# Kernel tuning notes

Measured on AMD Instinct MI355X. Metric: run time of the kernel, lower is better.

Reference implementation:

```python
import jax, jax.numpy as jnp
import numpy as np

MAX_EDGE_LENGTH = 100.0  # filtration cap from cfg['self_supervised']['max_edge_length']


def pairwise_dist(x):
    # Euclidean pairwise distances, [N, N]
    sq = jnp.sum(x * x, axis=-1)
    d2 = sq[:, None] + sq[None, :] - 2.0 * (x @ x.T)
    return jnp.sqrt(jnp.maximum(d2, 0.0) + 1e-12)


def mst_edge_weights(D):
    """Prim's MST over dense distance matrix D [N,N]. Returns N-1 edge weights.
    These weights are exactly the H0 death times of the Vietoris-Rips filtration
    (all H0 features are born at 0)."""
    N = D.shape[0]
    dist0 = D[0]                                   # min distance from tree to each node
    in_tree0 = jnp.zeros((N,), bool).at[0].set(True)

    def step(carry, _):
        dist, in_tree = carry
        masked = jnp.where(in_tree, jnp.inf, dist)
        j = jnp.argmin(masked)
        w = masked[j]                              # weight of edge added to MST
        in_tree = in_tree.at[j].set(True)
        dist = jnp.minimum(dist, D[j])
        return (dist, in_tree), w

    _, weights = jax.lax.scan(step, (dist0, in_tree0), None, length=N - 1)
    return weights


def h0_deaths(x):
    # H0 persistence diagram deaths (births are all 0), capped at max_edge_length
    return jnp.minimum(mst_edge_weights(pairwise_dist(x)), MAX_EDGE_LENGTH)


def setup_inputs() -> dict:
    key = jax.random.key(0)
    k1, k2 = jax.random.split(key)
    N, Dm = 4096, 128
    x_1 = jax.random.normal(k1, (N, Dm), dtype=jnp.float32)
    # correlated second view, as in a siamese/self-supervised setting
    x_2 = x_1 + 0.1 * jax.random.normal(k2, (N, Dm), dtype=jnp.float32)
    return {"x_1": x_1, "x_2": x_2, "plot": 0}


def reference(x_1, x_2, plot):
    # MSE representation loss
    representation_loss = jnp.mean((x_1 - x_2) ** 2)
    # H0 persistence diagrams via Vietoris-Rips (MST formulation)
    d1 = jnp.sort(h0_deaths(x_1))
    d2 = jnp.sort(h0_deaths(x_2))
    # Wasserstein-1 distance between the two H0 diagrams (births all 0,
    # equal cardinality => optimal matching is the sorted matching of deaths)
    topological_loss = jnp.sum(jnp.abs(d1 - d2))
    return representation_loss + topological_loss
```

## Files before the change

### kernel.cpp

```cpp
#include <hip/hip_runtime.h>
#include <hip/hip_fp16.h>

#define NPT 4096
#define DM 128
#define ROUNDS 12
#define INF64 0xFFFFFFFFFFFFFFFFull

typedef _Float16 f16x8 __attribute__((ext_vector_type(8)));
typedef _Float16 f16x2 __attribute__((ext_vector_type(2)));
typedef float f32x4 __attribute__((ext_vector_type(4)));

__global__ __launch_bounds__(256) void init_kernel(unsigned* __restrict__ comp,
                                                   unsigned long long* __restrict__ compbest,
                                                   float* __restrict__ w,
                                                   unsigned* __restrict__ cnt,
                                                   float* __restrict__ rep) {
    int i = blockIdx.x * blockDim.x + threadIdx.x;
    comp[i] = (unsigned)(i & (NPT - 1));
    compbest[i] = INF64;
    w[i] = 0.0f;
    if (i < 2) cnt[i] = 0u;
    if (i == 0) rep[0] = 0.0f;
}

__global__ __launch_bounds__(256) void prep_kernel(const float* __restrict__ x1,
                                                   const float* __restrict__ x2,
                                                   _Float16* __restrict__ Xh,
                                                   float* __restrict__ norms) {
    const int wv = threadIdx.x >> 6, ln = threadIdx.x & 63;
    const int row = blockIdx.x * 4 + wv;
    const float* src = (row < NPT) ? (x1 + (size_t)row * DM)
                                   : (x2 + (size_t)(row - NPT) * DM);
    float2 v = *(const float2*)(src + ln * 2);
    _Float16 h0 = (_Float16)v.x, h1 = (_Float16)v.y;
    f16x2 p; p[0] = h0; p[1] = h1;
    *(f16x2*)(Xh + (size_t)row * DM + ln * 2) = p;
    float a = (float)h0, b = (float)h1;
    float s = a * a + b * b;
    #pragma unroll
    for (int off = 32; off > 0; off >>= 1) s += __shfl_down(s, off);
    if (ln == 0) norms[row] = s;
}

__global__ __launch_bounds__(256) void gram_kernel(const _Float16* __restrict__ Xh,
                                                   const float* __restrict__ norms,
                                                   __half* __restrict__ Dall) {
    const int mat = blockIdx.y;
    const _Float16* __restrict__ X = Xh + (size_t)mat * NPT * DM;
    const float* __restrict__ nrm = norms + mat * NPT;
    __half* __restrict__ D = Dall + (size_t)mat * NPT * NPT;

    const int I = blockIdx.x >> 5;
    const int J = blockIdx.x & 31;

    __shared__ _Float16 tile[128 * 136];

    const int t = threadIdx.x;
    const int wv = t >> 6, ln = t & 63;
    const int rloc = (wv >> 1) * 64;
    const int cloc = (wv & 1) * 64;
    const int rowBase = I * 128 + rloc;
    const int colBase = J * 128 + cloc;
    const int lr = ln & 15;
    const int kg = ln >> 4;

    f32x4 acc[4][4];
    #pragma unroll
    for (int m = 0; m < 4; ++m)
        #pragma unroll
        for (int n = 0; n < 4; ++n)
            acc[m][n] = (f32x4){0.f, 0.f, 0.f, 0.f};

    #pragma unroll
    for (int ks = 0; ks < 4; ++ks) {
        const int k0 = ks * 32 + kg * 8;
        f16x8 a[4], b[4];
        #pragma unroll
        for (int m = 0; m < 4; ++m)
            a[m] = *(const f16x8*)(X + (size_t)(rowBase + m * 16 + lr) * DM + k0);
        #pragma unroll
        for (int n = 0; n < 4; ++n)
            b[n] = *(const f16x8*)(X + (size_t)(colBase + n * 16 + lr) * DM + k0);
        #pragma unroll
        for (int m = 0; m < 4; ++m)
            #pragma unroll
            for (int n = 0; n < 4; ++n)
                acc[m][n] = __builtin_amdgcn_mfma_f32_16x16x32_f16(a[m], b[n], acc[m][n], 0, 0, 0);
    }

    float nr[16], nc[4];
    #pragma unroll
    for (int m = 0; m < 4; ++m)
        #pragma unroll
        for (int q = 0; q < 4; ++q)
            nr[m * 4 + q] = nrm[rowBase + m * 16 + kg * 4 + q];
    #pragma unroll
    for (int n = 0; n < 4; ++n) nc[n] = nrm[colBase + n * 16 + lr];

    #pragma unroll
    for (int m = 0; m < 4; ++m) {
        #pragma unroll
        for (int n = 0; n < 4; ++n) {
            #pragma unroll
            for (int q = 0; q < 4; ++q) {
                const int rl = rloc + m * 16 + kg * 4 + q;
                const int cl = cloc + n * 16 + lr;
                float d2 = nr[m * 4 + q] + nc[n] - 2.0f * acc[m][n][q];
                float d = sqrtf(fmaxf(d2, 0.0f) + 1e-12f);
                tile[rl * 136 + cl] = (_Float16)d;
            }
        }
    }
    __syncthreads();

    const int tileRow0 = I * 128;
    #pragma unroll
    for (int it = 0; it < 8; ++it) {
        int idx = it * 256 + t;
        int row = idx >> 4;
        int ch = idx & 15;
        *(uint4*)(&D[(size_t)(tileRow0 + row) * NPT + J * 128 + ch * 8]) =
            *(const uint4*)(&tile[row * 136 + ch * 8]);
    }
}

__global__ __launch_bounds__(1024) void boruvka_a(const __half* __restrict__ Dall,
                                                  const unsigned* __restrict__ compAll,
                                                  unsigned long long* __restrict__ compbestAll,
                                                  const unsigned* __restrict__ cnt) {
    const int mat = blockIdx.y;
    if (cnt[mat] >= NPT - 1u) return;
    const __half* __restrict__ D = Dall + (size_t)mat * NPT * NPT;
    const unsigned* __restrict__ comp = compAll + mat * NPT;
    unsigned long long* __restrict__ compbest = compbestAll + mat * NPT;

    __shared__ unsigned short lcomp[NPT];
    const int t = threadIdx.x;
    for (int i = t; i < NPT; i += 1024) lcomp[i] = (unsigned short)comp[i];
    __syncthreads();

    const int wv = t >> 6, ln = t & 63;
    const int node = blockIdx.x * 16 + wv;
    const unsigned ci = lcomp[node];
    const unsigned* __restrict__ row = (const unsigned*)(D + (size_t)node * NPT);

    unsigned best = 0xFFFFFFFFu;
    #pragma unroll
    for (int k = 0; k < 8; ++k) {
        const int jb = k * 512 + ln * 8;
        uint4 dv = *(const uint4*)(row + (jb >> 1));
        uint4 cv = *(const uint4*)&lcomp[jb];
        const unsigned dp[4] = {dv.x, dv.y, dv.z, dv.w};
        const unsigned cp[4] = {cv.x, cv.y, cv.z, cv.w};
        #pragma unroll
        for (int q = 0; q < 4; ++q) {
            int j0 = jb + q * 2;
            unsigned k0 = (dp[q] << 16) | (unsigned)j0;
            unsigned k1 = (dp[q] & 0xFFFF0000u) | (unsigned)(j0 + 1);
            if ((cp[q] & 0xFFFFu) == ci) k0 = 0xFFFFFFFFu;
            if ((cp[q] >> 16) == ci)     k1 = 0xFFFFFFFFu;
            unsigned m = k0 < k1 ? k0 : k1;
            best = best < m ? best : m;
        }
    }
    #pragma unroll
    for (int off = 32; off > 0; off >>= 1) {
        unsigned o = __shfl_down(best, off);
        best = best < o ? best : o;
    }
    if (ln == 0 && best != 0xFFFFFFFFu) {
        unsigned h = best >> 16;
        unsigned j = best & 0xFFFFu;
        unsigned mn = (unsigned)node < j ? (unsigned)node : j;
        unsigned mx = (unsigned)node < j ? j : (unsigned)node;
        unsigned long long key64 = ((unsigned long long)h << 48) |
                                   ((unsigned long long)mn << 32) |
                                   ((unsigned long long)mx << 16) |
                                   (unsigned long long)j;
        atomicMin(&compbest[ci], key64);
    }
}

__global__ __launch_bounds__(1024) void boruvka_cd(unsigned* __restrict__ compAll,
                                                   unsigned long long* __restrict__ compbestAll,
                                                   float* __restrict__ wAll,
                                                   unsigned* __restrict__ cntAll) {
    const int mat = blockIdx.x;
    if (cntAll[mat] >= NPT - 1u) return;
    unsigned* __restrict__ comp = compAll + mat * NPT;
    unsigned long long* __restrict__ compbest = compbestAll + mat * NPT;
    float* __restrict__ w = wAll + mat * NPT;
    unsigned* __restrict__ cnt = cntAll + mat;

    __shared__ unsigned short par[NPT];
    const int t = threadIdx.x;

    for (int c = t; c < NPT; c += 1024) {
        unsigned p = (unsigned)c;
        unsigned long long key = compbest[c];
        if (comp[c] == (unsigned)c && key != INF64) {
            unsigned jout = (unsigned)(key & 0xFFFFull);
            unsigned c2 = comp[jout];
            unsigned long long k2 = compbest[c2];
            bool mutual = (k2 >> 16) == (key >> 16);
            if (!mutual || (unsigned)c < c2) {
                unsigned short hb = (unsigned short)(key >> 48);
                float wv = fminf(__half2float(__ushort_as_half(hb)), 100.0f);
                unsigned slot = atomicAdd(cnt, 1u);
                w[slot] = wv;
            }
            p = (mutual && (unsigned)c < c2) ? (unsigned)c : c2;
        }
        par[c] = (unsigned short)p;
    }
    __syncthreads();

    for (int it = 0; it < 12; ++it) {
        unsigned short np[4];
        #pragma unroll
        for (int q = 0; q < 4; ++q) np[q] = par[par[t + q * 1024]];
        __syncthreads();
        #pragma unroll
        for (int q = 0; q < 4; ++q) par[t + q * 1024] = np[q];
        __syncthreads();
    }

    for (int c = t; c < NPT; c += 1024) {
        comp[c] = par[comp[c]];
        compbest[c] = INF64;
    }
}

__global__ __launch_bounds__(256) void rep_kernel(const float4* __restrict__ x1,
                                                  const float4* __restrict__ x2,
                                                  float* __restrict__ acc) {
    int idx = blockIdx.x * blockDim.x + threadIdx.x;
    int stride = gridDim.x * blockDim.x;
    float s = 0.f;
    for (int i = idx; i < NPT * DM / 4; i += stride) {
        float4 a = x1[i], b = x2[i];
        float d0 = a.x - b.x, d1 = a.y - b.y, d2 = a.z - b.z, d3 = a.w - b.w;
        s += d0 * d0 + d1 * d1 + d2 * d2 + d3 * d3;
    }
    #pragma unroll
    for (int off = 32; off > 0; off >>= 1) s += __shfl_down(s, off);
    __shared__ float partial[4];
    int wv = threadIdx.x >> 6, ln = threadIdx.x & 63;
    if (ln == 0) partial[wv] = s;
    __syncthreads();
    if (threadIdx.x == 0) {
        float tot = partial[0] + partial[1] + partial[2] + partial[3];
        atomicAdd(acc, tot);
    }
}

__global__ __launch_bounds__(1024) void sort_kernel(float* __restrict__ wAll) {
    float* __restrict__ w = wAll + blockIdx.x * NPT;
    __shared__ float s[NPT];
    const int t = threadIdx.x;
    for (int i = t; i < NPT; i += 1024) s[i] = w[i];
    __syncthreads();

    for (int k = 2; k <= NPT; k <<= 1) {
        for (int j = k >> 1; j > 0; j >>= 1) {
            for (int i = t; i < NPT; i += 1024) {
                int ixj = i ^ j;
                if (ixj > i) {
                    bool up = (i & k) == 0;
                    float a = s[i], b = s[ixj];
                    if ((a > b) == up) { s[i] = b; s[ixj] = a; }
                }
            }
            __syncthreads();
        }
    }
    for (int i = t; i < NPT; i += 1024) w[i] = s[i];
}

__global__ __launch_bounds__(1024) void final2_kernel(const float* __restrict__ w,
                                                      const float* __restrict__ rep,
                                                      float* __restrict__ out) {
    const int t = threadIdx.x;
    float loc = 0.f;
    for (int i = t; i < NPT; i += 1024) loc += fabsf(w[i] - w[NPT + i]);
    #pragma unroll
    for (int off = 32; off > 0; off >>= 1) loc += __shfl_down(loc, off);
    __shared__ float reds[16];
    int wv = t >> 6, ln = t & 63;
    if (ln == 0) reds[wv] = loc;
    __syncthreads();
    if (t == 0) {
        float tot = 0.f;
        #pragma unroll
        for (int i = 0; i < 16; ++i) tot += reds[i];
        out[0] = tot + rep[0] * (1.0f / (NPT * DM));
    }
}

extern "C" void kernel_launch(void* const* d_in, const int* in_sizes, int n_in,
                              void* d_out, int out_size, void* d_ws, size_t ws_size,
                              hipStream_t stream) {
    const float* x1 = (const float*)d_in[0];
    const float* x2 = (const float*)d_in[1];
    float* out = (float*)d_out;

    char* ws = (char*)d_ws;
    __half* D = (__half*)ws;
    size_t off = (size_t)2 * NPT * NPT * sizeof(__half);
    _Float16* Xh = (_Float16*)(ws + off);
    off += (size_t)2 * NPT * DM * sizeof(_Float16);
    float* norms = (float*)(ws + off);
    off += (size_t)2 * NPT * sizeof(float);
    unsigned long long* compbest = (unsigned long long*)(ws + off);
    off += (size_t)2 * NPT * sizeof(unsigned long long);
    float* w = (float*)(ws + off);
    off += (size_t)2 * NPT * sizeof(float);
    unsigned* comp = (unsigned*)(ws + off);
    off += (size_t)2 * NPT * sizeof(unsigned);
    unsigned* cnt = (unsigned*)(ws + off);
    off += 4 * sizeof(unsigned);
    float* rep = (float*)(ws + off);

    init_kernel<<<2 * NPT / 256, 256, 0, stream>>>(comp, compbest, w, cnt, rep);

    prep_kernel<<<2 * NPT / 4, 256, 0, stream>>>(x1, x2, Xh, norms);

    gram_kernel<<<dim3(1024, 2), 256, 0, stream>>>(Xh, norms, D);

    for (int r = 0; r < ROUNDS; ++r) {
        boruvka_a<<<dim3(NPT / 16, 2), 1024, 0, stream>>>(D, comp, compbest, cnt);
        boruvka_cd<<<2, 1024, 0, stream>>>(comp, compbest, w, cnt);
    }

    rep_kernel<<<256, 256, 0, stream>>>((const float4*)x1, (const float4*)x2, rep);

    sort_kernel<<<2, 1024, 0, stream>>>(w);

    final2_kernel<<<1, 1024, 0, stream>>>(w, rep, out);
}
```

Baseline: 340.5 us.

## Cache per-node top-8 neighbors and finish Boruvka rounds in one persistent block per matrix

The first Boruvka pass now keeps each node's eight nearest neighbors in a per-node cache instead of only the single best edge. The remaining rounds run inside one block per matrix, which uses the cache to find each component's cheapest outgoing edge. A node rescans its full distance row only when all eight cached neighbors already lie in its own component. This replaces 12 full-matrix scan rounds and 24 launches with one scan plus mostly cache lookups. The cost is that later rounds run on only two workgroups, which could serialize work if many nodes fall back to full rescans.

```diff
diff --git a/kernel.cpp b/kernel.cpp
--- a/kernel.cpp
+++ b/kernel.cpp
@@ -3,12 +3,20 @@
 
 #define NPT 4096
 #define DM 128
-#define ROUNDS 12
 #define INF64 0xFFFFFFFFFFFFFFFFull
+#define INF32 0xFFFFFFFFu
 
 typedef _Float16 f16x8 __attribute__((ext_vector_type(8)));
 typedef _Float16 f16x2 __attribute__((ext_vector_type(2)));
 typedef float f32x4 __attribute__((ext_vector_type(4)));
+
+static __device__ __forceinline__ unsigned long long make_key64(unsigned key, unsigned node) {
+    unsigned h = key >> 16, j = key & 0xFFFFu;
+    unsigned mn = node < j ? node : j;
+    unsigned mx = node < j ? j : node;
+    return ((unsigned long long)h << 48) | ((unsigned long long)mn << 32) |
+           ((unsigned long long)mx << 16) | (unsigned long long)j;
+}
 
 __global__ __launch_bounds__(256) void init_kernel(unsigned* __restrict__ comp,
                                                    unsigned long long* __restrict__ compbest,
@@ -124,61 +132,80 @@
     }
 }
 
-__global__ __launch_bounds__(1024) void boruvka_a(const __half* __restrict__ Dall,
-                                                  const unsigned* __restrict__ compAll,
-                                                  unsigned long long* __restrict__ compbestAll,
-                                                  const unsigned* __restrict__ cnt) {
+__global__ __launch_bounds__(1024) void boruvka0(const __half* __restrict__ Dall,
+                                                 unsigned* __restrict__ cacheAll,
+                                                 unsigned long long* __restrict__ compbestAll) {
     const int mat = blockIdx.y;
-    if (cnt[mat] >= NPT - 1u) return;
     const __half* __restrict__ D = Dall + (size_t)mat * NPT * NPT;
-    const unsigned* __restrict__ comp = compAll + mat * NPT;
+    unsigned* __restrict__ cache = cacheAll + (size_t)mat * NPT * 8;
     unsigned long long* __restrict__ compbest = compbestAll + mat * NPT;
 
-    __shared__ unsigned short lcomp[NPT];
-    const int t = threadIdx.x;
-    for (int i = t; i < NPT; i += 1024) lcomp[i] = (unsigned short)comp[i];
-    __syncthreads();
-
-    const int wv = t >> 6, ln = t & 63;
+    const int t = threadIdx.x, wv = t >> 6, ln = t & 63;
     const int node = blockIdx.x * 16 + wv;
-    const unsigned ci = lcomp[node];
     const unsigned* __restrict__ row = (const unsigned*)(D + (size_t)node * NPT);
 
-    unsigned best = 0xFFFFFFFFu;
+    unsigned k8[8];
+    #pragma unroll
+    for (int s = 0; s < 8; ++s) k8[s] = INF32;
+
     #pragma unroll
     for (int k = 0; k < 8; ++k) {
         const int jb = k * 512 + ln * 8;
         uint4 dv = *(const uint4*)(row + (jb >> 1));
-        uint4 cv = *(const uint4*)&lcomp[jb];
         const unsigned dp[4] = {dv.x, dv.y, dv.z, dv.w};
-        const unsigned cp[4] = {cv.x, cv.y, cv.z, cv.w};
         #pragma unroll
         for (int q = 0; q < 4; ++q) {
             int j0 = jb + q * 2;
-            unsigned k0 = (dp[q] << 16) | (unsigned)j0;
-            unsigned k1 = (dp[q] & 0xFFFF0000u) | (unsigned)(j0 + 1);
-            if ((cp[q] & 0xFFFFu) == ci) k0 = 0xFFFFFFFFu;
-            if ((cp[q] >> 16) == ci)     k1 = 0xFFFFFFFFu;
-            unsigned m = k0 < k1 ? k0 : k1;
-            best = best < m ? best : m;
-        }
-    }
-    #pragma unroll
-    for (int off = 32; off > 0; off >>= 1) {
-        unsigned o = __shfl_down(best, off);
-        best = best < o ? best : o;
-    }
-    if (ln == 0 && best != 0xFFFFFFFFu) {
-        unsigned h = best >> 16;
-        unsigned j = best & 0xFFFFu;
-        unsigned mn = (unsigned)node < j ? (unsigned)node : j;
-        unsigned mx = (unsigned)node < j ? j : (unsigned)node;
-        unsigned long long key64 = ((unsigned long long)h << 48) |
-                                   ((unsigned long long)mn << 32) |
-                                   ((unsigned long long)mx << 16) |
-                                   (unsigned long long)j;
-        atomicMin(&compbest[ci], key64);
-    }
+            unsigned kk0 = (dp[q] << 16) | (unsigned)j0;
+            unsigned kk1 = (dp[q] & 0xFFFF0000u) | (unsigned)(j0 + 1);
+            if (j0 == node) kk0 = INF32;
+            if (j0 + 1 == node) kk1 = INF32;
+            if (kk0 < k8[7]) {
+                unsigned cur = kk0;
+                #pragma unroll
+                for (int s = 0; s < 8; ++s) {
+                    unsigned mn = cur < k8[s] ? cur : k8[s];
+                    unsigned mx = cur < k8[s] ? k8[s] : cur;
+                    k8[s] = mn; cur = mx;
+                }
+            }
+            if (kk1 < k8[7]) {
+                unsigned cur = kk1;
+                #pragma unroll
+                for (int s = 0; s < 8; ++s) {
+                    unsigned mn = cur < k8[s] ? cur : k8[s];
+                    unsigned mx = cur < k8[s] ? k8[s] : cur;
+                    k8[s] = mn; cur = mx;
+                }
+            }
+        }
+    }
+
+    #pragma unroll
+    for (int off = 1; off < 64; off <<= 1) {
+        unsigned b[8], c[8];
+        #pragma unroll
+        for (int s = 0; s < 8; ++s) b[s] = __shfl_xor(k8[s], off);
+        #pragma unroll
+        for (int s = 0; s < 8; ++s) {
+            unsigned x = k8[s], y = b[7 - s];
+            c[s] = x < y ? x : y;
+        }
+        #define CE(i, j) { unsigned mn = c[i] < c[j] ? c[i] : c[j]; \
+                           unsigned mx = c[i] < c[j] ? c[j] : c[i]; c[i] = mn; c[j] = mx; }
+        CE(0,4) CE(1,5) CE(2,6) CE(3,7)
+        CE(0,2) CE(1,3) CE(4,6) CE(5,7)
+        CE(0,1) CE(2,3) CE(4,5) CE(6,7)
+        #undef CE
+        #pragma unroll
+        for (int s = 0; s < 8; ++s) k8[s] = c[s];
+    }
+
+    unsigned sel = k8[0];
+    #pragma unroll
+    for (int s = 1; s < 8; ++s) sel = (ln == s) ? k8[s] : sel;
+    if (ln < 8) cache[(size_t)node * 8 + ln] = sel;
+    if (ln == 0) compbest[node] = make_key64(k8[0], (unsigned)node);
 }
 
 __global__ __launch_bounds__(1024) void boruvka_cd(unsigned* __restrict__ compAll,
@@ -186,7 +213,6 @@
                                                    float* __restrict__ wAll,
                                                    unsigned* __restrict__ cntAll) {
     const int mat = blockIdx.x;
-    if (cntAll[mat] >= NPT - 1u) return;
     unsigned* __restrict__ comp = compAll + mat * NPT;
     unsigned long long* __restrict__ compbest = compbestAll + mat * NPT;
     float* __restrict__ w = wAll + mat * NPT;
@@ -225,9 +251,125 @@
         __syncthreads();
     }
 
-    for (int c = t; c < NPT; c += 1024) {
-        comp[c] = par[comp[c]];
-        compbest[c] = INF64;
+    for (int c = t; c < NPT; c += 1024) comp[c] = par[comp[c]];
+}
+
+__global__ __launch_bounds__(1024) void mst_finish(const __half* __restrict__ Dall,
+                                                   const unsigned* __restrict__ cacheAll,
+                                                   const unsigned* __restrict__ compAll,
+                                                   float* __restrict__ wAll,
+                                                   const unsigned* __restrict__ cntAll) {
+    const int mat = blockIdx.x;
+    const __half* __restrict__ D = Dall + (size_t)mat * NPT * NPT;
+    const unsigned* __restrict__ cache = cacheAll + (size_t)mat * NPT * 8;
+    const unsigned* __restrict__ comp = compAll + mat * NPT;
+    float* __restrict__ w = wAll + mat * NPT;
+
+    __shared__ unsigned short lcomp[NPT];
+    __shared__ unsigned short par[NPT];
+    __shared__ unsigned long long cbest[NPT];
+    __shared__ unsigned short flist[NPT];
+    __shared__ unsigned counters[2];
+
+    const int t = threadIdx.x, wv = t >> 6, ln = t & 63;
+    for (int i = t; i < NPT; i += 1024) lcomp[i] = (unsigned short)comp[i];
+    unsigned cnt = cntAll[mat];
+    __syncthreads();
+
+    for (int round = 0; round < 20; ++round) {
+        if (cnt >= NPT - 1u) break;
+
+        for (int i = t; i < NPT; i += 1024) cbest[i] = INF64;
+        if (t == 0) { counters[0] = 0u; counters[1] = 0u; }
+        __syncthreads();
+
+        for (int nd = t; nd < NPT; nd += 1024) {
+            uint4 c0 = *(const uint4*)(cache + (size_t)nd * 8);
+            uint4 c1 = *(const uint4*)(cache + (size_t)nd * 8 + 4);
+            const unsigned e[8] = {c0.x, c0.y, c0.z, c0.w, c1.x, c1.y, c1.z, c1.w};
+            const unsigned ci = lcomp[nd];
+            unsigned found = INF32;
+            #pragma unroll
+            for (int q = 0; q < 8; ++q) {
+                if (found == INF32 && lcomp[e[q] & 0xFFFFu] != ci) found = e[q];
+            }
+            if (found != INF32)
+                atomicMin(&cbest[ci], make_key64(found, (unsigned)nd));
+            else
+                flist[atomicAdd(&counters[0], 1u)] = (unsigned short)nd;
+        }
+        __syncthreads();
+
+        const unsigned nf = counters[0];
+        for (unsigned fi = (unsigned)wv; fi < nf; fi += 16) {
+            const int node = flist[fi];
+            const unsigned ci = lcomp[node];
+            const unsigned* __restrict__ row = (const unsigned*)(D + (size_t)node * NPT);
+            unsigned best = INF32;
+            #pragma unroll
+            for (int k = 0; k < 8; ++k) {
+                const int jb = k * 512 + ln * 8;
+                uint4 dv = *(const uint4*)(row + (jb >> 1));
+                uint4 cv = *(const uint4*)&lcomp[jb];
+                const unsigned dp[4] = {dv.x, dv.y, dv.z, dv.w};
+                const unsigned cp[4] = {cv.x, cv.y, cv.z, cv.w};
+                #pragma unroll
+                for (int q = 0; q < 4; ++q) {
+                    int j0 = jb + q * 2;
+                    unsigned kk0 = (dp[q] << 16) | (unsigned)j0;
+                    unsigned kk1 = (dp[q] & 0xFFFF0000u) | (unsigned)(j0 + 1);
+                    if ((cp[q] & 0xFFFFu) == ci) kk0 = INF32;
+                    if ((cp[q] >> 16) == ci)     kk1 = INF32;
+                    unsigned m = kk0 < kk1 ? kk0 : kk1;
+                    best = best < m ? best : m;
+                }
+            }
+            #pragma unroll
+            for (int off = 32; off > 0; off >>= 1) {
+                unsigned o = __shfl_down(best, off);
+                best = best < o ? best : o;
+            }
+            if (ln == 0 && best != INF32)
+                atomicMin(&cbest[ci], make_key64(best, (unsigned)node));
+        }
+        __syncthreads();
+
+        for (int c = t; c < NPT; c += 1024) {
+            unsigned p = (unsigned)c;
+            if (lcomp[c] == (unsigned short)c) {
+                unsigned long long key = cbest[c];
+                if (key != INF64) {
+                    unsigned jout = (unsigned)(key & 0xFFFFull);
+                    unsigned c2 = lcomp[jout];
+                    unsigned long long k2 = cbest[c2];
+                    bool mutual = (k2 >> 16) == (key >> 16);
+                    if (!mutual || (unsigned)c < c2) {
+                        unsigned short hb = (unsigned short)(key >> 48);
+                        float wvv = fminf(__half2float(__ushort_as_half(hb)), 100.0f);
+                        unsigned slot = atomicAdd(&counters[1], 1u);
+                        w[cnt + slot] = wvv;
+                    }
+                    p = (mutual && (unsigned)c < c2) ? (unsigned)c : c2;
+                }
+            }
+            par[c] = (unsigned short)p;
+        }
+        __syncthreads();
+
+        for (int it = 0; it < 12; ++it) {
+            unsigned short np[4];
+            #pragma unroll
+            for (int q = 0; q < 4; ++q) np[q] = par[par[t + q * 1024]];
+            __syncthreads();
+            #pragma unroll
+            for (int q = 0; q < 4; ++q) par[t + q * 1024] = np[q];
+            __syncthreads();
+        }
+
+        for (int c = t; c < NPT; c += 1024) lcomp[c] = par[lcomp[c]];
+        __syncthreads();
+        cnt += counters[1];
+        __syncthreads();
     }
 }
 
@@ -317,8 +459,10 @@
     off += (size_t)2 * NPT * sizeof(float);
     unsigned* comp = (unsigned*)(ws + off);
     off += (size_t)2 * NPT * sizeof(unsigned);
+    unsigned* cache = (unsigned*)(ws + off);
+    off += (size_t)2 * NPT * 8 * sizeof(unsigned);
     unsigned* cnt = (unsigned*)(ws + off);
-    off += 4 * sizeof(unsigned);
+    off += 2 * sizeof(unsigned);
     float* rep = (float*)(ws + off);
 
     init_kernel<<<2 * NPT / 256, 256, 0, stream>>>(comp, compbest, w, cnt, rep);
@@ -327,10 +471,11 @@
 
     gram_kernel<<<dim3(1024, 2), 256, 0, stream>>>(Xh, norms, D);
 
-    for (int r = 0; r < ROUNDS; ++r) {
-        boruvka_a<<<dim3(NPT / 16, 2), 1024, 0, stream>>>(D, comp, compbest, cnt);
-        boruvka_cd<<<2, 1024, 0, stream>>>(comp, compbest, w, cnt);
-    }
+    boruvka0<<<dim3(NPT / 16, 2), 1024, 0, stream>>>(D, cache, compbest);
+
+    boruvka_cd<<<2, 1024, 0, stream>>>(comp, compbest, w, cnt);
+
+    mst_finish<<<2, 1024, 0, stream>>>(D, cache, comp, w, cnt);
 
     rep_kernel<<<256, 256, 0, stream>>>((const float4*)x1, (const float4*)x2, rep);
 
```

New measurement: 996.3 us. 2.93x slower.

## Fuse first Boruvka round into gram kernel and MSE into prep

Applied to the files above, without the earlier changes.

The gram kernel now computes each row's nearest neighbour within its tile while writing distances, and atomically seeds compbest, which replaces the first boruvka_a pass over the full distance matrix. The representation MSE is folded into prep_kernel, so rep_kernel and its extra read of the inputs are gone. boruvka_a2 now handles two rows per wavefront, sharing the component loads from LDS. The costs are extra shuffles and atomics in the gram epilogue and higher register pressure in the Boruvka kernel.

```diff
diff --git a/kernel.cpp b/kernel.cpp
--- a/kernel.cpp
+++ b/kernel.cpp
@@ -5,10 +5,19 @@
 #define DM 128
 #define ROUNDS 12
 #define INF64 0xFFFFFFFFFFFFFFFFull
+#define INF32 0xFFFFFFFFu
 
 typedef _Float16 f16x8 __attribute__((ext_vector_type(8)));
 typedef _Float16 f16x2 __attribute__((ext_vector_type(2)));
 typedef float f32x4 __attribute__((ext_vector_type(4)));
+
+static __device__ __forceinline__ unsigned long long make_key64(unsigned key, unsigned node) {
+    unsigned h = key >> 16, j = key & 0xFFFFu;
+    unsigned mn = node < j ? node : j;
+    unsigned mx = node < j ? j : node;
+    return ((unsigned long long)h << 48) | ((unsigned long long)mn << 32) |
+           ((unsigned long long)mx << 16) | (unsigned long long)j;
+}
 
 __global__ __launch_bounds__(256) void init_kernel(unsigned* __restrict__ comp,
                                                    unsigned long long* __restrict__ compbest,
@@ -26,34 +35,54 @@
 __global__ __launch_bounds__(256) void prep_kernel(const float* __restrict__ x1,
                                                    const float* __restrict__ x2,
                                                    _Float16* __restrict__ Xh,
-                                                   float* __restrict__ norms) {
+                                                   float* __restrict__ norms,
+                                                   float* __restrict__ rep) {
     const int wv = threadIdx.x >> 6, ln = threadIdx.x & 63;
     const int row = blockIdx.x * 4 + wv;
-    const float* src = (row < NPT) ? (x1 + (size_t)row * DM)
-                                   : (x2 + (size_t)(row - NPT) * DM);
-    float2 v = *(const float2*)(src + ln * 2);
-    _Float16 h0 = (_Float16)v.x, h1 = (_Float16)v.y;
-    f16x2 p; p[0] = h0; p[1] = h1;
-    *(f16x2*)(Xh + (size_t)row * DM + ln * 2) = p;
-    float a = (float)h0, b = (float)h1;
-    float s = a * a + b * b;
-    #pragma unroll
-    for (int off = 32; off > 0; off >>= 1) s += __shfl_down(s, off);
-    if (ln == 0) norms[row] = s;
+    float2 v1 = *(const float2*)(x1 + (size_t)row * DM + ln * 2);
+    float2 v2 = *(const float2*)(x2 + (size_t)row * DM + ln * 2);
+    _Float16 a0 = (_Float16)v1.x, a1 = (_Float16)v1.y;
+    _Float16 b0 = (_Float16)v2.x, b1 = (_Float16)v2.y;
+    f16x2 pa; pa[0] = a0; pa[1] = a1;
+    f16x2 pb; pb[0] = b0; pb[1] = b1;
+    *(f16x2*)(Xh + (size_t)row * DM + ln * 2) = pa;
+    *(f16x2*)(Xh + (size_t)(NPT + row) * DM + ln * 2) = pb;
+
+    float s1 = (float)a0 * (float)a0 + (float)a1 * (float)a1;
+    float s2 = (float)b0 * (float)b0 + (float)b1 * (float)b1;
+    float dx = v1.x - v2.x, dy = v1.y - v2.y;
+    float rs = dx * dx + dy * dy;
+    #pragma unroll
+    for (int off = 32; off > 0; off >>= 1) {
+        s1 += __shfl_down(s1, off);
+        s2 += __shfl_down(s2, off);
+        rs += __shfl_down(rs, off);
+    }
+    __shared__ float partial[4];
+    if (ln == 0) {
+        norms[row] = s1;
+        norms[NPT + row] = s2;
+        partial[wv] = rs;
+    }
+    __syncthreads();
+    if (threadIdx.x == 0)
+        atomicAdd(rep, partial[0] + partial[1] + partial[2] + partial[3]);
 }
 
 __global__ __launch_bounds__(256) void gram_kernel(const _Float16* __restrict__ Xh,
                                                    const float* __restrict__ norms,
-                                                   __half* __restrict__ Dall) {
+                                                   __half* __restrict__ Dall,
+                                                   unsigned long long* __restrict__ compbestAll) {
     const int mat = blockIdx.y;
     const _Float16* __restrict__ X = Xh + (size_t)mat * NPT * DM;
     const float* __restrict__ nrm = norms + mat * NPT;
     __half* __restrict__ D = Dall + (size_t)mat * NPT * NPT;
+    unsigned long long* __restrict__ compbest = compbestAll + mat * NPT;
 
     const int I = blockIdx.x >> 5;
     const int J = blockIdx.x & 31;
 
-    __shared__ _Float16 tile[128 * 136];
+    __shared__ __half tile[128 * 136];
 
     const int t = threadIdx.x;
     const int wv = t >> 6, ln = t & 63;
@@ -100,15 +129,29 @@
     #pragma unroll
     for (int m = 0; m < 4; ++m) {
         #pragma unroll
-        for (int n = 0; n < 4; ++n) {
+        for (int q = 0; q < 4; ++q) {
+            const int rl = rloc + m * 16 + kg * 4 + q;
+            const int rglob = I * 128 + rl;
+            unsigned best = INF32;
             #pragma unroll
-            for (int q = 0; q < 4; ++q) {
-                const int rl = rloc + m * 16 + kg * 4 + q;
+            for (int n = 0; n < 4; ++n) {
                 const int cl = cloc + n * 16 + lr;
+                const int cglob = J * 128 + cl;
                 float d2 = nr[m * 4 + q] + nc[n] - 2.0f * acc[m][n][q];
                 float d = sqrtf(fmaxf(d2, 0.0f) + 1e-12f);
-                tile[rl * 136 + cl] = (_Float16)d;
+                __half hd = __float2half(d);
+                tile[rl * 136 + cl] = hd;
+                unsigned key = ((unsigned)__half_as_ushort(hd) << 16) | (unsigned)cglob;
+                if (cglob == rglob) key = INF32;
+                best = best < key ? best : key;
             }
+            #pragma unroll
+            for (int off2 = 1; off2 < 16; off2 <<= 1) {
+                unsigned o = __shfl_xor(best, off2);
+                best = best < o ? best : o;
+            }
+            if (lr == 0)
+                atomicMin(&compbest[rglob], make_key64(best, (unsigned)rglob));
         }
     }
     __syncthreads();
@@ -124,10 +167,10 @@
     }
 }
 
-__global__ __launch_bounds__(1024) void boruvka_a(const __half* __restrict__ Dall,
-                                                  const unsigned* __restrict__ compAll,
-                                                  unsigned long long* __restrict__ compbestAll,
-                                                  const unsigned* __restrict__ cnt) {
+__global__ __launch_bounds__(1024) void boruvka_a2(const __half* __restrict__ Dall,
+                                                   const unsigned* __restrict__ compAll,
+                                                   unsigned long long* __restrict__ compbestAll,
+                                                   const unsigned* __restrict__ cnt) {
     const int mat = blockIdx.y;
     if (cnt[mat] >= NPT - 1u) return;
     const __half* __restrict__ D = Dall + (size_t)mat * NPT * NPT;
@@ -140,44 +183,51 @@
     __syncthreads();
 
     const int wv = t >> 6, ln = t & 63;
-    const int node = blockIdx.x * 16 + wv;
-    const unsigned ci = lcomp[node];
-    const unsigned* __restrict__ row = (const unsigned*)(D + (size_t)node * NPT);
-
-    unsigned best = 0xFFFFFFFFu;
+    const int node0 = blockIdx.x * 32 + wv * 2;
+    const int node1 = node0 + 1;
+    const unsigned ci0 = lcomp[node0];
+    const unsigned ci1 = lcomp[node1];
+    const unsigned* __restrict__ row0 = (const unsigned*)(D + (size_t)node0 * NPT);
+    const unsigned* __restrict__ row1 = row0 + (NPT / 2);
+
+    unsigned best0 = INF32, best1 = INF32;
     #pragma unroll
     for (int k = 0; k < 8; ++k) {
         const int jb = k * 512 + ln * 8;
-        uint4 dv = *(const uint4*)(row + (jb >> 1));
+        uint4 dv0 = *(const uint4*)(row0 + (jb >> 1));
+        uint4 dv1 = *(const uint4*)(row1 + (jb >> 1));
         uint4 cv = *(const uint4*)&lcomp[jb];
-        const unsigned dp[4] = {dv.x, dv.y, dv.z, dv.w};
-        const unsigned cp[4] = {cv.x, cv.y, cv.z, cv.w};
+        const unsigned dp0[4] = {dv0.x, dv0.y, dv0.z, dv0.w};
+        const unsigned dp1[4] = {dv1.x, dv1.y, dv1.z, dv1.w};
+        const unsigned cp[4]  = {cv.x, cv.y, cv.z, cv.w};
         #pragma unroll
         for (int q = 0; q < 4; ++q) {
             int j0 = jb + q * 2;
-            unsigned k0 = (dp[q] << 16) | (unsigned)j0;
-            unsigned k1 = (dp[q] & 0xFFFF0000u) | (unsigned)(j0 + 1);
-            if ((cp[q] & 0xFFFFu) == ci) k0 = 0xFFFFFFFFu;
-            if ((cp[q] >> 16) == ci)     k1 = 0xFFFFFFFFu;
-            unsigned m = k0 < k1 ? k0 : k1;
-            best = best < m ? best : m;
+            unsigned clo = cp[q] & 0xFFFFu, chi = cp[q] >> 16;
+            unsigned k00 = (dp0[q] << 16) | (unsigned)j0;
+            unsigned k01 = (dp0[q] & 0xFFFF0000u) | (unsigned)(j0 + 1);
+            if (clo == ci0) k00 = INF32;
+            if (chi == ci0) k01 = INF32;
+            unsigned m0 = k00 < k01 ? k00 : k01;
+            best0 = best0 < m0 ? best0 : m0;
+            unsigned k10 = (dp1[q] << 16) | (unsigned)j0;
+            unsigned k11 = (dp1[q] & 0xFFFF0000u) | (unsigned)(j0 + 1);
+            if (clo == ci1) k10 = INF32;
+            if (chi == ci1) k11 = INF32;
+            unsigned m1 = k10 < k11 ? k10 : k11;
+            best1 = best1 < m1 ? best1 : m1;
         }
     }
     #pragma unroll
     for (int off = 32; off > 0; off >>= 1) {
-        unsigned o = __shfl_down(best, off);
-        best = best < o ? best : o;
-    }
-    if (ln == 0 && best != 0xFFFFFFFFu) {
-        unsigned h = best >> 16;
-        unsigned j = best & 0xFFFFu;
-        unsigned mn = (unsigned)node < j ? (unsigned)node : j;
-        unsigned mx = (unsigned)node < j ? j : (unsigned)node;
-        unsigned long long key64 = ((unsigned long long)h << 48) |
-                                   ((unsigned long long)mn << 32) |
-                                   ((unsigned long long)mx << 16) |
-                                   (unsigned long long)j;
-        atomicMin(&compbest[ci], key64);
+        unsigned o0 = __shfl_down(best0, off);
+        best0 = best0 < o0 ? best0 : o0;
+        unsigned o1 = __shfl_down(best1, off);
+        best1 = best1 < o1 ? best1 : o1;
+    }
+    if (ln == 0) {
+        if (best0 != INF32) atomicMin(&compbest[ci0], make_key64(best0, (unsigned)node0));
+        if (best1 != INF32) atomicMin(&compbest[ci1], make_key64(best1, (unsigned)node1));
     }
 }
 
@@ -231,29 +281,6 @@
     }
 }
 
-__global__ __launch_bounds__(256) void rep_kernel(const float4* __restrict__ x1,
-                                                  const float4* __restrict__ x2,
-                                                  float* __restrict__ acc) {
-    int idx = blockIdx.x * blockDim.x + threadIdx.x;
-    int stride = gridDim.x * blockDim.x;
-    float s = 0.f;
-    for (int i = idx; i < NPT * DM / 4; i += stride) {
-        float4 a = x1[i], b = x2[i];
-        float d0 = a.x - b.x, d1 = a.y - b.y, d2 = a.z - b.z, d3 = a.w - b.w;
-        s += d0 * d0 + d1 * d1 + d2 * d2 + d3 * d3;
-    }
-    #pragma unroll
-    for (int off = 32; off > 0; off >>= 1) s += __shfl_down(s, off);
-    __shared__ float partial[4];
-    int wv = threadIdx.x >> 6, ln = threadIdx.x & 63;
-    if (ln == 0) partial[wv] = s;
-    __syncthreads();
-    if (threadIdx.x == 0) {
-        float tot = partial[0] + partial[1] + partial[2] + partial[3];
-        atomicAdd(acc, tot);
-    }
-}
-
 __global__ __launch_bounds__(1024) void sort_kernel(float* __restrict__ wAll) {
     float* __restrict__ w = wAll + blockIdx.x * NPT;
     __shared__ float s[NPT];
@@ -318,22 +345,22 @@
     unsigned* comp = (unsigned*)(ws + off);
     off += (size_t)2 * NPT * sizeof(unsigned);
     unsigned* cnt = (unsigned*)(ws + off);
-    off += 4 * sizeof(unsigned);
+    off += 2 * sizeof(unsigned);
     float* rep = (float*)(ws + off);
 
     init_kernel<<<2 * NPT / 256, 256, 0, stream>>>(comp, compbest, w, cnt, rep);
 
-    prep_kernel<<<2 * NPT / 4, 256, 0, stream>>>(x1, x2, Xh, norms);
-
-    gram_kernel<<<dim3(1024, 2), 256, 0, stream>>>(Xh, norms, D);
-
-    for (int r = 0; r < ROUNDS; ++r) {
-        boruvka_a<<<dim3(NPT / 16, 2), 1024, 0, stream>>>(D, comp, compbest, cnt);
+    prep_kernel<<<NPT / 4, 256, 0, stream>>>(x1, x2, Xh, norms, rep);
+
+    gram_kernel<<<dim3(1024, 2), 256, 0, stream>>>(Xh, norms, D, compbest);
+
+    boruvka_cd<<<2, 1024, 0, stream>>>(comp, compbest, w, cnt);
+
+    for (int r = 1; r < ROUNDS; ++r) {
+        boruvka_a2<<<dim3(NPT / 32, 2), 1024, 0, stream>>>(D, comp, compbest, cnt);
         boruvka_cd<<<2, 1024, 0, stream>>>(comp, compbest, w, cnt);
     }
 
-    rep_kernel<<<256, 256, 0, stream>>>((const float4*)x1, (const float4*)x2, rep);
-
     sort_kernel<<<2, 1024, 0, stream>>>(w);
 
     final2_kernel<<<1, 1024, 0, stream>>>(w, rep, out);
```

Result: slower. 363.5 us (+6.7%).
